# Performance work log

Measured on AMD Instinct MI355X. Metric: run time of the kernel, lower is better.

## Reference

```python
import jax, jax.numpy as jnp
import numpy as np

# Network topology constants (topological order: inputs, L hidden layers, outputs)
N_IN = 512
H = 1024      # hidden nodes per layer
L = 8         # hidden layers
N_OUT = 256
DEG = 64      # enabled incoming connections per non-input node
B = 1024      # batch of input vectors

LAYER_SIZES = [H] * L + [N_OUT]
E_TOTAL = sum(n * DEG for n in LAYER_SIZES)  # 540672


def setup_inputs() -> dict:
    key = jax.random.key(0)
    k_in, k_w = jax.random.split(key)
    inputs = jax.random.normal(k_in, (B, N_IN), dtype=jnp.float32)
    # scale weights ~1/sqrt(DEG) so sigmoid pre-activations are well-conditioned
    weights = jax.random.normal(k_w, (E_TOTAL,), dtype=jnp.float32) / np.sqrt(DEG)
    # src indices: for each layer, incoming edges may come from ANY earlier node
    rng = np.random.default_rng(0)
    src_chunks = []
    n_before = N_IN
    for n in LAYER_SIZES:
        src_chunks.append(rng.integers(0, n_before, size=n * DEG))
        n_before += n
    src_idx = jnp.asarray(np.concatenate(src_chunks), dtype=jnp.int32)
    return {"inputs": inputs, "weights": weights, "src_idx": src_idx}


def reference(inputs, weights, src_idx):
    # outs: [B, n_nodes_evaluated_so_far], grown layer by layer (topological order)
    outs = inputs
    off = 0
    for n in LAYER_SIZES:
        e = n * DEG
        s = src_idx[off:off + e]            # [e] gather indices into earlier nodes
        w = weights[off:off + e]            # [e]
        gathered = outs[:, s] * w           # [B, e] irregular gather + scale
        z = gathered.reshape(-1, n, DEG).sum(-1)  # per-node sum over DEG in-edges
        outs = jnp.concatenate([outs, jax.nn.sigmoid(z)], axis=1)
        off += e
    return outs[:, -N_OUT:]  # [B, N_OUT] outputs of 'output' nodes
```

## Files before the change

kernel.cpp:

```cpp
#include <hip/hip_runtime.h>
#include <math.h>


#define N_IN    512
#define NLAYER  9
#define DEG     64
#define BATCH   1024
#define BPB     4
#define THREADS 1024
#define TOTAL_N 8960
#define N_OUT   256
#define NEDGE_N 8448

union H4 { uint2 u; _Float16 h[4]; };
union H2 { unsigned u; _Float16 h[2]; };
union HS { _Float16 h; unsigned short s; };

__device__ __forceinline__ int jswz(int i) {
    return (i & ~15) | ((i + (i >> 4)) & 15);
}

__global__ __launch_bounds__(256)
void neat_prep(const float* __restrict__ wts,
               const int*   __restrict__ sidx,
               uint4*       __restrict__ rec)
{
    __shared__ unsigned sortbuf[4][64];

    const int tid  = threadIdx.x;
    const int wave = tid >> 6;
    const int lane = tid & 63;
    const int t    = blockIdx.x * 4 + wave;
    const unsigned long long lt = (1ull << lane) - 1ull;

    const int e   = (t << 6) + lane;
    const int idx = sidx[e];
    HS w; w.h = (_Float16)wts[e];
    const int cA = idx & 15;
    const int cB = (idx + (idx >> 4)) & 15;

    unsigned long long mA[16];
    #pragma unroll
    for (int cc = 0; cc < 16; ++cc) mA[cc] = __ballot(cA == cc);
    const int rankA = (int)__popcll(mA[cA] & lt);
    const bool accA = rankA < 4;

    unsigned long long mB[16];
    #pragma unroll
    for (int cc = 0; cc < 16; ++cc) mB[cc] = __ballot(!accA && cB == cc);
    int uAcB = (int)__popcll(mA[cB]); uAcB = uAcB < 4 ? uAcB : 4;
    const int rankB = (int)__popcll(mB[cB] & lt);
    const bool accB = !accA && (rankB < 4 - uAcB);

    const bool placed = accA || accB;
    int slot_pre;
    if (placed) {
        slot_pre = accA ? ((cA << 2) + rankA) : ((cB << 2) + uAcB + rankB);
    } else {
        const unsigned long long msp = __ballot(!placed);
        const int myspill = (int)__popcll(msp & lt);
        int hcum = 0; slot_pre = 0;
        bool found = false;
        #pragma unroll
        for (int cc = 0; cc < 16; ++cc) {
            int uA = (int)__popcll(mA[cc]); uA = uA < 4 ? uA : 4;
            int uB = (int)__popcll(mB[cc]); const int capB = 4 - uA;
            uB = uB < capB ? uB : capB;
            const int used  = uA + uB;
            const int holes = 4 - used;
            const bool take = !found && (myspill < hcum + holes);
            slot_pre = take ? ((cc << 2) + used + (myspill - hcum)) : slot_pre;
            found = found || take;
            hcum += holes;
        }
    }

    const int v = accB ? (8960 + jswz(idx)) : idx;

    const int fl    = t & 63;
    const int sigma = ((fl & 15) << 2) | (fl >> 4);
    const int slot  = (slot_pre + sigma) & 63;
    sortbuf[wave][slot] = (unsigned)v | ((unsigned)w.s << 16);
    __syncthreads();

    if (lane < 16) {
        const unsigned s0 = sortbuf[wave][(lane << 2) + 0];
        const unsigned s1 = sortbuf[wave][(lane << 2) + 1];
        const unsigned s2 = sortbuf[wave][(lane << 2) + 2];
        const unsigned s3 = sortbuf[wave][(lane << 2) + 3];
        uint4 o;
        o.x = (s0 & 0xffffu) | (s1 << 16);
        o.y = (s2 & 0xffffu) | (s3 << 16);
        o.z = (s0 >> 16) | (s1 & 0xffff0000u);
        o.w = (s2 >> 16) | (s3 & 0xffff0000u);
        rec[((t >> 6) << 10) + (lane << 6) + fl] = o;
    }
}

__global__ __launch_bounds__(THREADS, 4)
void neat_fwd(const float* __restrict__ in,
              const uint4* __restrict__ rec,
              float*       __restrict__ out)
{
    __shared__ _Float16 act[2 * TOTAL_N * BPB];

    const int tid   = threadIdx.x;
    const int bbase = blockIdx.x * BPB;

    {
        const float* src = in + bbase * N_IN;
        for (int t = tid; t < BPB * N_IN; t += THREADS) {
            int j = t >> 9;
            int i = t & (N_IN - 1);
            const _Float16 v = (_Float16)src[t];
            act[(i << 2) + j] = v;
            act[((8960 + jswz(i)) << 2) + j] = v;
        }
    }
    __syncthreads();

    int recBase = 0;
    int nb      = N_IN;
    #pragma unroll 1
    for (int layer = 0; layer < NLAYER; ++layer) {
        const int n = (layer < NLAYER - 1) ? 1024 : N_OUT;
        if (tid < n) {
            const int neuron = tid;
            const uint4* rp = rec + recBase + ((neuron >> 6) << 10) + (neuron & 63);

            uint4 r[16];
            #pragma unroll
            for (int q = 0; q < 16; ++q) r[q] = rp[q << 6];

            float accx = 0.f, accy = 0.f, accz = 0.f, accw = 0.f;
            #pragma unroll
            for (int q = 0; q < 16; ++q) {
                const uint4 r4 = r[q];
                H4 g0, g1, g2, g3;
                g0.u = *reinterpret_cast<const uint2*>(act + ((r4.x & 0xffffu) << 2));
                g1.u = *reinterpret_cast<const uint2*>(act + ((r4.x >> 16) << 2));
                g2.u = *reinterpret_cast<const uint2*>(act + ((r4.y & 0xffffu) << 2));
                g3.u = *reinterpret_cast<const uint2*>(act + ((r4.y >> 16) << 2));
                H2 wz, ww; wz.u = r4.z; ww.u = r4.w;
                const float w0 = (float)wz.h[0];
                const float w1 = (float)wz.h[1];
                const float w2 = (float)ww.h[0];
                const float w3 = (float)ww.h[1];
                accx = fmaf((float)g0.h[0], w0, accx);
                accy = fmaf((float)g0.h[1], w0, accy);
                accz = fmaf((float)g0.h[2], w0, accz);
                accw = fmaf((float)g0.h[3], w0, accw);
                accx = fmaf((float)g1.h[0], w1, accx);
                accy = fmaf((float)g1.h[1], w1, accy);
                accz = fmaf((float)g1.h[2], w1, accz);
                accw = fmaf((float)g1.h[3], w1, accw);
                accx = fmaf((float)g2.h[0], w2, accx);
                accy = fmaf((float)g2.h[1], w2, accy);
                accz = fmaf((float)g2.h[2], w2, accz);
                accw = fmaf((float)g2.h[3], w2, accw);
                accx = fmaf((float)g3.h[0], w3, accx);
                accy = fmaf((float)g3.h[1], w3, accy);
                accz = fmaf((float)g3.h[2], w3, accz);
                accw = fmaf((float)g3.h[3], w3, accw);
            }

            float4 sg;
            sg.x = 1.f / (1.f + __expf(-accx));
            sg.y = 1.f / (1.f + __expf(-accy));
            sg.z = 1.f / (1.f + __expf(-accz));
            sg.w = 1.f / (1.f + __expf(-accw));

            if (layer < NLAYER - 1) {
                H4 p;
                p.h[0] = (_Float16)sg.x; p.h[1] = (_Float16)sg.y;
                p.h[2] = (_Float16)sg.z; p.h[3] = (_Float16)sg.w;
                const int no = nb + neuron;
                *reinterpret_cast<uint2*>(act + (no << 2)) = p.u;
                *reinterpret_cast<uint2*>(act + ((8960 + jswz(no)) << 2)) = p.u;
            } else {
                float* op = out + neuron;
                op[(bbase + 0) * N_OUT] = sg.x;
                op[(bbase + 1) * N_OUT] = sg.y;
                op[(bbase + 2) * N_OUT] = sg.z;
                op[(bbase + 3) * N_OUT] = sg.w;
            }
        }
        __syncthreads();
        recBase += n << 4;
        nb      += n;
    }
}

extern "C" void kernel_launch(void* const* d_in, const int* in_sizes, int n_in,
                              void* d_out, int out_size, void* d_ws, size_t ws_size,
                              hipStream_t stream)
{
    const float* in  = (const float*)d_in[0];
    const float* wts = (const float*)d_in[1];
    const int*   sx  = (const int*)d_in[2];
    float*       out = (float*)d_out;
    uint4*       rec = (uint4*)d_ws;

    neat_prep<<<NEDGE_N / 4, 256, 0, stream>>>(wts, sx, rec);
    neat_fwd<<<BATCH / BPB, THREADS, 0, stream>>>(in, rec, out);
}
```

Before: 51.68 us.

## Drop bank-aware edge sorting and duplicated swizzled activation table

The prep kernel becomes a plain per-record repack: it loads four source indices and four weights with vector loads and converts the weights to half precision. It no longer runs the ballot-based sort that placed edges into LDS bank slots. The forward kernel keeps a single activation table, which halves its shared memory and removes the second swizzled store per activation. The aim is a cheaper prep pass and fewer LDS writes. In exchange, the random gathers in the forward pass can hit more shared-memory bank conflicts.

Result: faster. 48.46 us (-6.2%).

```diff
diff --git a/kernel.cpp b/kernel.cpp
--- a/kernel.cpp
+++ b/kernel.cpp
@@ -10,91 +10,36 @@
 #define THREADS 1024
 #define TOTAL_N 8960
 #define N_OUT   256
-#define NEDGE_N 8448
+#define NREC    135168
 
 union H4 { uint2 u; _Float16 h[4]; };
 union H2 { unsigned u; _Float16 h[2]; };
 union HS { _Float16 h; unsigned short s; };
-
-__device__ __forceinline__ int jswz(int i) {
-    return (i & ~15) | ((i + (i >> 4)) & 15);
-}
 
 __global__ __launch_bounds__(256)
 void neat_prep(const float* __restrict__ wts,
                const int*   __restrict__ sidx,
                uint4*       __restrict__ rec)
 {
-    __shared__ unsigned sortbuf[4][64];
+    const int r = blockIdx.x * 256 + threadIdx.x;
+    const int l = r >> 14;
+    const int j = r & 16383;
+    const int n = ((j >> 10) << 6) | (j & 63);
+    const int q = (j >> 6) & 15;
+    const int e0 = (l << 16) + (n << 6) + (q << 2);
 
-    const int tid  = threadIdx.x;
-    const int wave = tid >> 6;
-    const int lane = tid & 63;
-    const int t    = blockIdx.x * 4 + wave;
-    const unsigned long long lt = (1ull << lane) - 1ull;
+    const int4   s4 = *reinterpret_cast<const int4*>(sidx + e0);
+    const float4 w4 = *reinterpret_cast<const float4*>(wts + e0);
+    HS h0, h1, h2, h3;
+    h0.h = (_Float16)w4.x; h1.h = (_Float16)w4.y;
+    h2.h = (_Float16)w4.z; h3.h = (_Float16)w4.w;
 
-    const int e   = (t << 6) + lane;
-    const int idx = sidx[e];
-    HS w; w.h = (_Float16)wts[e];
-    const int cA = idx & 15;
-    const int cB = (idx + (idx >> 4)) & 15;
-
-    unsigned long long mA[16];
-    #pragma unroll
-    for (int cc = 0; cc < 16; ++cc) mA[cc] = __ballot(cA == cc);
-    const int rankA = (int)__popcll(mA[cA] & lt);
-    const bool accA = rankA < 4;
-
-    unsigned long long mB[16];
-    #pragma unroll
-    for (int cc = 0; cc < 16; ++cc) mB[cc] = __ballot(!accA && cB == cc);
-    int uAcB = (int)__popcll(mA[cB]); uAcB = uAcB < 4 ? uAcB : 4;
-    const int rankB = (int)__popcll(mB[cB] & lt);
-    const bool accB = !accA && (rankB < 4 - uAcB);
-
-    const bool placed = accA || accB;
-    int slot_pre;
-    if (placed) {
-        slot_pre = accA ? ((cA << 2) + rankA) : ((cB << 2) + uAcB + rankB);
-    } else {
-        const unsigned long long msp = __ballot(!placed);
-        const int myspill = (int)__popcll(msp & lt);
-        int hcum = 0; slot_pre = 0;
-        bool found = false;
-        #pragma unroll
-        for (int cc = 0; cc < 16; ++cc) {
-            int uA = (int)__popcll(mA[cc]); uA = uA < 4 ? uA : 4;
-            int uB = (int)__popcll(mB[cc]); const int capB = 4 - uA;
-            uB = uB < capB ? uB : capB;
-            const int used  = uA + uB;
-            const int holes = 4 - used;
-            const bool take = !found && (myspill < hcum + holes);
-            slot_pre = take ? ((cc << 2) + used + (myspill - hcum)) : slot_pre;
-            found = found || take;
-            hcum += holes;
-        }
-    }
-
-    const int v = accB ? (8960 + jswz(idx)) : idx;
-
-    const int fl    = t & 63;
-    const int sigma = ((fl & 15) << 2) | (fl >> 4);
-    const int slot  = (slot_pre + sigma) & 63;
-    sortbuf[wave][slot] = (unsigned)v | ((unsigned)w.s << 16);
-    __syncthreads();
-
-    if (lane < 16) {
-        const unsigned s0 = sortbuf[wave][(lane << 2) + 0];
-        const unsigned s1 = sortbuf[wave][(lane << 2) + 1];
-        const unsigned s2 = sortbuf[wave][(lane << 2) + 2];
-        const unsigned s3 = sortbuf[wave][(lane << 2) + 3];
-        uint4 o;
-        o.x = (s0 & 0xffffu) | (s1 << 16);
-        o.y = (s2 & 0xffffu) | (s3 << 16);
-        o.z = (s0 >> 16) | (s1 & 0xffff0000u);
-        o.w = (s2 >> 16) | (s3 & 0xffff0000u);
-        rec[((t >> 6) << 10) + (lane << 6) + fl] = o;
-    }
+    uint4 o;
+    o.x = ((unsigned)s4.x & 0xffffu) | ((unsigned)s4.y << 16);
+    o.y = ((unsigned)s4.z & 0xffffu) | ((unsigned)s4.w << 16);
+    o.z = (unsigned)h0.s | ((unsigned)h1.s << 16);
+    o.w = (unsigned)h2.s | ((unsigned)h3.s << 16);
+    rec[r] = o;
 }
 
 __global__ __launch_bounds__(THREADS, 4)
@@ -102,7 +47,7 @@
               const uint4* __restrict__ rec,
               float*       __restrict__ out)
 {
-    __shared__ _Float16 act[2 * TOTAL_N * BPB];
+    __shared__ _Float16 act[TOTAL_N * BPB];
 
     const int tid   = threadIdx.x;
     const int bbase = blockIdx.x * BPB;
@@ -112,9 +57,7 @@
         for (int t = tid; t < BPB * N_IN; t += THREADS) {
             int j = t >> 9;
             int i = t & (N_IN - 1);
-            const _Float16 v = (_Float16)src[t];
-            act[(i << 2) + j] = v;
-            act[((8960 + jswz(i)) << 2) + j] = v;
+            act[i * BPB + j] = (_Float16)src[t];
         }
     }
     __syncthreads();
@@ -174,9 +117,7 @@
                 H4 p;
                 p.h[0] = (_Float16)sg.x; p.h[1] = (_Float16)sg.y;
                 p.h[2] = (_Float16)sg.z; p.h[3] = (_Float16)sg.w;
-                const int no = nb + neuron;
-                *reinterpret_cast<uint2*>(act + (no << 2)) = p.u;
-                *reinterpret_cast<uint2*>(act + ((8960 + jswz(no)) << 2)) = p.u;
+                *reinterpret_cast<uint2*>(act + ((nb + neuron) << 2)) = p.u;
             } else {
                 float* op = out + neuron;
                 op[(bbase + 0) * N_OUT] = sg.x;
@@ -201,6 +142,6 @@
     float*       out = (float*)d_out;
     uint4*       rec = (uint4*)d_ws;
 
-    neat_prep<<<NEDGE_N / 4, 256, 0, stream>>>(wts, sx, rec);
+    neat_prep<<<NREC / 256, 256, 0, stream>>>(wts, sx, rec);
     neat_fwd<<<BATCH / BPB, THREADS, 0, stream>>>(in, rec, out);
 }
```
